# Kernel optimization log

Measured on AMD Instinct MI355X. Metric: run time of the kernel, lower is better.

## Reference

```python
import jax, jax.numpy as jnp
from jax import lax
import numpy as np

V, E, H, B, T = 512, 512, 1024, 128, 512

def _xavier(key, shape):
    fan_out, fan_in = shape
    bound = float(np.sqrt(6.0 / (fan_in + fan_out)))
    return jax.random.uniform(key, shape, jnp.float32, -bound, bound)

def setup_inputs() -> dict:
    key = jax.random.key(0)
    ks = jax.random.split(key, 6)
    src = jax.random.randint(ks[0], (B, T), 0, V, dtype=jnp.int32)
    embedding = _xavier(ks[1], (V, E))
    w_ih_l0 = _xavier(ks[2], (3 * H, E))
    w_hh_l0 = _xavier(ks[3], (3 * H, H))
    w_ih_l1 = _xavier(ks[4], (3 * H, H))
    w_hh_l1 = _xavier(ks[5], (3 * H, H))
    zb = jnp.zeros((3 * H,), jnp.float32)  # biases init'd to 0 in module
    return {
        "src": src, "embedding": embedding,
        "w_ih_l0": w_ih_l0, "w_hh_l0": w_hh_l0, "b_ih_l0": zb, "b_hh_l0": zb,
        "w_ih_l1": w_ih_l1, "w_hh_l1": w_hh_l1, "b_ih_l1": zb, "b_hh_l1": zb,
    }

def _gru_layer(x_seq, w_ih, w_hh, b_ih, b_hh):
    # x_seq: [B, T, D]. Precompute all input projections as one big GEMM.
    gates_x = jnp.einsum('btd,gd->btg', x_seq, w_ih) + b_ih  # [B, T, 3H]
    h_dim = w_hh.shape[1]
    w_hh_t = w_hh.T  # [H, 3H]

    def step(h, gx):
        gh = h @ w_hh_t + b_hh                      # [B, 3H]
        xr, xz, xn = jnp.split(gx, 3, axis=-1)
        hr, hz, hn = jnp.split(gh, 3, axis=-1)
        r = jax.nn.sigmoid(xr + hr)
        z = jax.nn.sigmoid(xz + hz)
        n = jnp.tanh(xn + r * hn)
        h_new = (1.0 - z) * n + z * h
        return h_new, h_new

    h0 = jnp.zeros((x_seq.shape[0], h_dim), x_seq.dtype)
    h_last, outs = lax.scan(step, h0, jnp.swapaxes(gates_x, 0, 1))  # time-major scan
    return jnp.swapaxes(outs, 0, 1), h_last  # [B, T, H], [B, H]

def reference(src, embedding, w_ih_l0, w_hh_l0, b_ih_l0, b_hh_l0,
              w_ih_l1, w_hh_l1, b_ih_l1, b_hh_l1):
    x = embedding[src]  # [B, T, E]
    y0, h0 = _gru_layer(x, w_ih_l0, w_hh_l0, b_ih_l0, b_hh_l0)
    _, h1 = _gru_layer(y0, w_ih_l1, w_hh_l1, b_ih_l1, b_hh_l1)
    return jnp.stack([h0, h1], axis=0)  # (n_layers, B, H)
```

## Files before the change

kernel.cpp:

```cpp
#include <hip/hip_runtime.h>

typedef __attribute__((ext_vector_type(8))) short short8;
typedef __attribute__((ext_vector_type(4))) float f32x4;

constexpr int Bsz = 128;
constexpr int Tlen = 512;
constexpr int Hd = 1024;
constexpr int RS = 128 * 1024;

__device__ __forceinline__ unsigned short f2b(float f) {
  unsigned int u = __float_as_uint(f);
  u = (u + 0x7FFFu + ((u >> 16) & 1u)) >> 16;
  return (unsigned short)u;
}
__device__ __forceinline__ unsigned int aload32(const unsigned int* p) {
  return __hip_atomic_load(p, __ATOMIC_RELAXED, __HIP_MEMORY_SCOPE_AGENT);
}
__device__ __forceinline__ void astore32(unsigned int* p, unsigned int v) {
  __hip_atomic_store(p, v, __ATOMIC_RELAXED, __HIP_MEMORY_SCOPE_AGENT);
}

template <int LAYER>
__device__ __forceinline__ void run_layer(
    const int* __restrict__ src, const float* __restrict__ P,
    const unsigned short* __restrict__ Wh, const unsigned short* __restrict__ Wx,
    const float* __restrict__ bhh, const float* __restrict__ bih,
    float* __restrict__ dout,
    unsigned short* __restrict__ A0r,
    unsigned short* __restrict__ A1hr,
    unsigned short* __restrict__ A1xr,
    unsigned int* __restrict__ flags,
    unsigned int* __restrict__ invflags,
    f32x4 (*__restrict__ red)[4][3][64],
    const int R0, const int J0, const int w, const int lane,
    const int tid, const int c, const int xcd, const bool isInv)
{
  constexpr int NQ = LAYER ? 4 : 3;
  const int lrow = lane >> 4;
  const int lcol = lane & 15;
  const int col = J0 + lcol;
  const int mh = R0 >> 6;
  const int dom = LAYER * 2 + mh;

  const float bhr = bhh[col], bhz = bhh[1024 + col], bhn = bhh[2048 + col];
  float gbr = 0.f, gbz = 0.f, gbn = 0.f;
  if (LAYER) { gbr = bih[col]; gbz = bih[1024 + col]; gbn = bih[2048 + col]; }

  short8 wBh[3][8];
#pragma unroll
  for (int g = 0; g < 3; ++g) {
    const unsigned short* wp = Wh + (g * 1024 + col) * 1024 + w * 256 + lrow * 8;
#pragma unroll
    for (int ks = 0; ks < 8; ++ks) wBh[g][ks] = *(const short8*)(wp + ks * 32);
  }
  short8 wBx[3][8];
  if (LAYER) {
#pragma unroll
    for (int g = 0; g < 3; ++g) {
      const unsigned short* wp = Wx + (g * 1024 + col) * 1024 + w * 256 + lrow * 8;
#pragma unroll
      for (int ks = 0; ks < 8; ++ks) wBx[g][ks] = *(const short8*)(wp + ks * 32);
    }
  }

  const int myrow0 = R0 + w * 16 + lrow * 4;
  float hold[4] = {0.f, 0.f, 0.f, 0.f};

  for (int r = 0; r <= 512; ++r) {
    if (LAYER == 0 && r == 512) break;
    const bool active = LAYER ? (r >= 1) : true;

    if (active) {
      const int scur = r & 3, snext = (r + 1) & 3;

      float gpr[4], gpz[4], gpn[4];
      if (LAYER == 0) {
        int sv[4];
#pragma unroll
        for (int i = 0; i < 4; ++i) sv[i] = src[(myrow0 + i) * Tlen + r];
#pragma unroll
        for (int i = 0; i < 4; ++i) {
          const float* pr = P + sv[i] * 3072 + col;
          gpr[i] = pr[0]; gpz[i] = pr[1024]; gpn[i] = pr[2048];
        }
      } else {
#pragma unroll
        for (int i = 0; i < 4; ++i) { gpr[i] = gbr; gpz[i] = gbz; gpn[i] = gbn; }
      }

      f32x4 ar[4], az[4], anh[4], anx[4];
#pragma unroll
      for (int f = 0; f < 4; ++f) {
        ar[f]  = (f32x4){0.f, 0.f, 0.f, 0.f};
        az[f]  = (f32x4){0.f, 0.f, 0.f, 0.f};
        anh[f] = (f32x4){0.f, 0.f, 0.f, 0.f};
        anx[f] = (f32x4){0.f, 0.f, 0.f, 0.f};
      }

      if (LAYER == 0) {
        if (r >= 1) {
          if (w == 0) {
            const unsigned tgt = (unsigned)r;
            if (isInv) {
              const unsigned tA = (r >= 2) ? (unsigned)(r - 2) : 0u;
              const unsigned int* f0 = flags + 0 * 64 + lane;
              const unsigned int* f1 = flags + 1 * 64 + lane;
              const unsigned int* f2 = flags + 2 * 64 + lane;
              const unsigned int* f3 = flags + 3 * 64 + lane;
              for (;;) {
                const unsigned a = aload32(f0), b = aload32(f1),
                               d = aload32(f2), e = aload32(f3);
                if (__all(a >= tgt && b >= tA && d >= tA && e >= tA)) break;
                __builtin_amdgcn_s_sleep(1);
              }
              __builtin_amdgcn_fence(__ATOMIC_ACQUIRE, "agent");
              if (lane == 0) astore32(&invflags[xcd * 16], (unsigned)(r + 1));
            } else {
              const unsigned int* fp = flags + mh * 64 + lane;
              const unsigned int* fs = flags + (2 + mh) * 64 + lane;
              const unsigned tgtS = (r >= 2) ? (unsigned)(r - 2) : 0u;
              const unsigned int* iv = &invflags[xcd * 16];
              for (;;) {
                const unsigned a = aload32(fp), b = aload32(fs), k = aload32(iv);
                if (__all(a >= tgt && b >= tgtS && k >= tgt)) break;
                __builtin_amdgcn_s_sleep(1);
              }
            }
          }
          __syncthreads();
          asm volatile("buffer_inv sc0" ::: "memory");

          const unsigned short* rb[4];
#pragma unroll
          for (int f = 0; f < 4; ++f)
            rb[f] = A0r + scur * RS + (R0 + f * 16 + lcol) * 1024 + w * 256 + lrow * 8;
          short8 ab[4][4];
#pragma unroll
          for (int s = 0; s < 4; ++s)
#pragma unroll
            for (int f = 0; f < 4; ++f) ab[s][f] = *(const short8*)(rb[f] + s * 32);
#pragma unroll
          for (int ks = 0; ks < 8; ++ks) {
#pragma unroll
            for (int f = 0; f < 4; ++f) {
              const short8 a = ab[ks & 3][f];
              ar[f]  = __builtin_amdgcn_mfma_f32_16x16x32_bf16(a, wBh[0][ks], ar[f], 0, 0, 0);
              az[f]  = __builtin_amdgcn_mfma_f32_16x16x32_bf16(a, wBh[1][ks], az[f], 0, 0, 0);
              anh[f] = __builtin_amdgcn_mfma_f32_16x16x32_bf16(a, wBh[2][ks], anh[f], 0, 0, 0);
            }
            if (ks + 4 < 8)
#pragma unroll
              for (int f = 0; f < 4; ++f)
                ab[ks & 3][f] = *(const short8*)(rb[f] + (ks + 4) * 32);
          }
        } else if (isInv) {
          if (w == 0 && lane == 0) astore32(&invflags[xcd * 16], 1u);
        }
      } else {
        if (w == 0) {
          const unsigned tgt = (unsigned)r;
          const unsigned int* fp = flags + mh * 64 + lane;
          const unsigned int* iv = &invflags[xcd * 16];
          for (;;) {
            const unsigned a = aload32(fp), k = aload32(iv);
            if (__all(a >= tgt && k >= tgt)) break;
            __builtin_amdgcn_s_sleep(1);
          }
        }
        __syncthreads();
        asm volatile("buffer_inv sc0" ::: "memory");
        {
          const unsigned short* rbx[4];
#pragma unroll
          for (int f = 0; f < 4; ++f)
            rbx[f] = A1xr + scur * RS + (R0 + f * 16 + lcol) * 1024 + w * 256 + lrow * 8;
          short8 ab[4][4];
#pragma unroll
          for (int s = 0; s < 4; ++s)
#pragma unroll
            for (int f = 0; f < 4; ++f) ab[s][f] = *(const short8*)(rbx[f] + s * 32);
#pragma unroll
          for (int ks = 0; ks < 8; ++ks) {
#pragma unroll
            for (int f = 0; f < 4; ++f) {
              const short8 a = ab[ks & 3][f];
              ar[f]  = __builtin_amdgcn_mfma_f32_16x16x32_bf16(a, wBx[0][ks], ar[f], 0, 0, 0);
              az[f]  = __builtin_amdgcn_mfma_f32_16x16x32_bf16(a, wBx[1][ks], az[f], 0, 0, 0);
              anx[f] = __builtin_amdgcn_mfma_f32_16x16x32_bf16(a, wBx[2][ks], anx[f], 0, 0, 0);
            }
            if (ks + 4 < 8)
#pragma unroll
              for (int f = 0; f < 4; ++f)
                ab[ks & 3][f] = *(const short8*)(rbx[f] + (ks + 4) * 32);
          }
        }
        if (r >= 2) {
          if (w == 0) {
            const unsigned tgt = (unsigned)r;
            const unsigned int* fs = flags + (2 + mh) * 64 + lane;
            for (;;) {
              const unsigned b = aload32(fs);
              if (__all(b >= tgt)) break;
              __builtin_amdgcn_s_sleep(1);
            }
          }
          __syncthreads();
          asm volatile("buffer_inv sc0" ::: "memory");
          const unsigned short* rbh[4];
#pragma unroll
          for (int f = 0; f < 4; ++f)
            rbh[f] = A1hr + scur * RS + (R0 + f * 16 + lcol) * 1024 + w * 256 + lrow * 8;
          short8 ab[4][4];
#pragma unroll
          for (int s = 0; s < 4; ++s)
#pragma unroll
            for (int f = 0; f < 4; ++f) ab[s][f] = *(const short8*)(rbh[f] + s * 32);
#pragma unroll
          for (int ks = 0; ks < 8; ++ks) {
#pragma unroll
            for (int f = 0; f < 4; ++f) {
              const short8 a = ab[ks & 3][f];
              ar[f]  = __builtin_amdgcn_mfma_f32_16x16x32_bf16(a, wBh[0][ks], ar[f], 0, 0, 0);
              az[f]  = __builtin_amdgcn_mfma_f32_16x16x32_bf16(a, wBh[1][ks], az[f], 0, 0, 0);
              anh[f] = __builtin_amdgcn_mfma_f32_16x16x32_bf16(a, wBh[2][ks], anh[f], 0, 0, 0);
            }
            if (ks + 4 < 8)
#pragma unroll
              for (int f = 0; f < 4; ++f)
                ab[ks & 3][f] = *(const short8*)(rbh[f] + (ks + 4) * 32);
          }
        }
      }

#pragma unroll
      for (int f = 0; f < 4; ++f) {
        if (f != w) {
          const int sl = (f < w) ? f : f - 1;
          red[w][0][sl][lane] = ar[f];
          red[w][1][sl][lane] = az[f];
          red[w][2][sl][lane] = anh[f];
          if (NQ == 4) red[w][3][sl][lane] = anx[f];
        }
      }
      __syncthreads();
      f32x4 sr  = (f32x4){0.f, 0.f, 0.f, 0.f};
      f32x4 sz_ = (f32x4){0.f, 0.f, 0.f, 0.f};
      f32x4 snh = (f32x4){0.f, 0.f, 0.f, 0.f};
      f32x4 snx = (f32x4){0.f, 0.f, 0.f, 0.f};
#pragma unroll
      for (int f = 0; f < 4; ++f)
        if (f == w) { sr = ar[f]; sz_ = az[f]; snh = anh[f]; if (NQ == 4) snx = anx[f]; }
#pragma unroll
      for (int ww = 0; ww < 4; ++ww) {
        if (ww != w) {
          const int sl = (w < ww) ? w : w - 1;
          sr  += red[ww][0][sl][lane];
          sz_ += red[ww][1][sl][lane];
          snh += red[ww][2][sl][lane];
          if (NQ == 4) snx += red[ww][3][sl][lane];
        }
      }

      const bool lastw = LAYER ? (r == 512) : (r == 511);
#pragma unroll
      for (int i = 0; i < 4; ++i) {
        const int row = myrow0 + i;
        float rg = sr[i] + gpr[i] + bhr;
        rg = 1.f / (1.f + __expf(-rg));
        float zg = sz_[i] + gpz[i] + bhz;
        zg = 1.f / (1.f + __expf(-zg));
        const float nx = (snx[i] + gpn[i]) + rg * (snh[i] + bhn);
        const float e2 = __expf(2.f * fabsf(nx));
        const float ng = copysignf(1.f - 2.f / (e2 + 1.f), nx);
        const float hnew = (1.f - zg) * ng + zg * hold[i];
        hold[i] = hnew;
        const unsigned int hb = (unsigned int)f2b(hnew);
        const unsigned int nb = (unsigned int)__shfl_down((int)hb, 1, 64);
        if ((lcol & 1) == 0) {
          const unsigned int pv = hb | (nb << 16);
          if (LAYER == 0) {
            astore32((unsigned int*)(A0r + snext * RS + row * 1024 + J0 + lcol), pv);
            astore32((unsigned int*)(A1xr + snext * RS + row * 1024 + J0 + lcol), pv);
          } else {
            astore32((unsigned int*)(A1hr + snext * RS + row * 1024 + J0 + lcol), pv);
          }
        }
        if (lastw) dout[LAYER * (Bsz * Hd) + row * Hd + col] = hnew;
      }
    }

    __syncthreads();
    if (tid == 0) astore32(&flags[dom * 64 + c], (unsigned)(r + 1));
  }
}

__global__ void __launch_bounds__(256, 1) gru_persist(
    const int* __restrict__ src,
    const float* __restrict__ P,
    const unsigned short* __restrict__ Whh0b,
    const unsigned short* __restrict__ Whh1b,
    const unsigned short* __restrict__ Wih1b,
    const float* __restrict__ bhh0,
    const float* __restrict__ bih1,
    const float* __restrict__ bhh1,
    float* __restrict__ dout,
    unsigned short* __restrict__ A0,
    unsigned short* __restrict__ A1h,
    unsigned short* __restrict__ A1x,
    unsigned int* __restrict__ flags,
    unsigned int* __restrict__ invflags,
    int* __restrict__ taken)
{
  __shared__ f32x4 red[4][4][3][64];
  __shared__ int s_work;

  const int tid = threadIdx.x;
  const int lane = tid & 63;

  if (tid == 0) {
    unsigned int xcc;
    asm volatile("s_getreg_b32 %0, hwreg(HW_REG_XCC_ID)" : "=s"(xcc));
    const int pref = ((int)(xcc & 7u)) * 32;
    int got = -1;
    for (int j = 0; j < 32 && got < 0; ++j) {
      const int idx = pref + j;
      int expected = 0;
      if (__hip_atomic_compare_exchange_strong(&taken[idx], &expected, 1,
              __ATOMIC_RELAXED, __ATOMIC_RELAXED, __HIP_MEMORY_SCOPE_AGENT))
        got = idx;
    }
    for (int j = 0; j < 256 && got < 0; ++j) {
      const int idx = (pref + j) & 255;
      int expected = 0;
      if (__hip_atomic_compare_exchange_strong(&taken[idx], &expected, 1,
              __ATOMIC_RELAXED, __ATOMIC_RELAXED, __HIP_MEMORY_SCOPE_AGENT))
        got = idx;
    }
    s_work = got;
  }
  __syncthreads();
  const int work = s_work;

  if (work < 0) {
    float h0 = 1.00f, h1 = 1.25f, h2 = 1.50f, h3 = 1.75f;
    float h4 = 2.00f, h5 = 2.25f, h6 = 2.50f, h7 = 2.75f;
    const float mm = 1.0000001f, ad = 0.0000003f;
    for (;;) {
#pragma unroll
      for (int i = 0; i < 256; ++i) {
        h0 = __builtin_fmaf(h0, mm, ad); h1 = __builtin_fmaf(h1, mm, ad);
        h2 = __builtin_fmaf(h2, mm, ad); h3 = __builtin_fmaf(h3, mm, ad);
        h4 = __builtin_fmaf(h4, mm, ad); h5 = __builtin_fmaf(h5, mm, ad);
        h6 = __builtin_fmaf(h6, mm, ad); h7 = __builtin_fmaf(h7, mm, ad);
      }
      asm volatile("" :: "v"(h0), "v"(h1), "v"(h2), "v"(h3),
                         "v"(h4), "v"(h5), "v"(h6), "v"(h7));
      const unsigned a = aload32(&flags[128 + lane]);
      const unsigned b = aload32(&flags[192 + lane]);
      if (__all(a >= 513u && b >= 513u)) break;
    }
    return;
  }

  const int xcd_w = work >> 5;
  const int slot = work & 31;
  const int layer = (slot >> 4) & 1;
  const int m = (slot >> 1) & 7;
  const int c = xcd_w * 8 + m;
  const int mh = slot & 1;
  const int R0 = mh * 64;
  const int J0 = c * 16;
  const bool isInv = (slot == 0);

  const int w = tid >> 6;

  if (layer == 0)
    run_layer<0>(src, P, Whh0b, Wih1b, bhh0, bih1, dout, A0, A1h, A1x,
                 flags, invflags, red, R0, J0, w, lane, tid, c, xcd_w, isInv);
  else
    run_layer<1>(src, P, Whh1b, Wih1b, bhh1, bih1, dout, A0, A1h, A1x,
                 flags, invflags, red, R0, J0, w, lane, tid, c, xcd_w, false);
}

__global__ void __launch_bounds__(256) cvt_k(const float* __restrict__ s,
                                            unsigned short* __restrict__ d, int n) {
  const int i = (blockIdx.x * 256 + threadIdx.x) * 8;
  if (i >= n) return;
  const float4 a = *(const float4*)(s + i);
  const float4 b = *(const float4*)(s + i + 4);
  short8 o;
  o[0] = (short)f2b(a.x); o[1] = (short)f2b(a.y);
  o[2] = (short)f2b(a.z); o[3] = (short)f2b(a.w);
  o[4] = (short)f2b(b.x); o[5] = (short)f2b(b.y);
  o[6] = (short)f2b(b.z); o[7] = (short)f2b(b.w);
  *(short8*)(d + i) = o;
}

__global__ void __launch_bounds__(256) pemb_k(const float* __restrict__ emb,
                                             const float* __restrict__ wih0,
                                             const float* __restrict__ bih0,
                                             float* __restrict__ P) {
  __shared__ float se[64 * 64];
  const int g = blockIdx.x * 256 + threadIdx.x;
  const int v0 = blockIdx.y * 64;
  float acc[64];
#pragma unroll
  for (int i = 0; i < 64; ++i) acc[i] = 0.f;
  for (int kb = 0; kb < 8; ++kb) {
    __syncthreads();
#pragma unroll
    for (int s = 0; s < 4; ++s) {
      const int idx = threadIdx.x + s * 256;
      const int vv = idx >> 4, k4 = (idx & 15) * 4;
      *(float4*)(se + vv * 64 + k4) =
          *(const float4*)(emb + (v0 + vv) * 512 + kb * 64 + k4);
    }
    __syncthreads();
    float4 wv[16];
#pragma unroll
    for (int j = 0; j < 16; ++j)
      wv[j] = *(const float4*)(wih0 + g * 512 + kb * 64 + j * 4);
    for (int vv = 0; vv < 64; ++vv) {
      const float* er = se + vv * 64;
      float s0 = acc[vv];
#pragma unroll
      for (int j = 0; j < 16; ++j) {
        const float4 e = *(const float4*)(er + j * 4);
        s0 += wv[j].x * e.x + wv[j].y * e.y + wv[j].z * e.z + wv[j].w * e.w;
      }
      acc[vv] = s0;
    }
  }
  const float bb = bih0[g];
  for (int vv = 0; vv < 64; ++vv) P[(v0 + vv) * 3072 + g] = acc[vv] + bb;
}

__global__ void zero_k(unsigned int* flags, int* taken, unsigned int* invflags) {
  const int i = threadIdx.x;
  flags[i] = 0u;
  taken[i] = 0;
  if (i < 128) invflags[i] = 0u;
}

extern "C" void kernel_launch(void* const* d_in, const int* in_sizes, int n_in,
                              void* d_out, int out_size, void* d_ws, size_t ws_size,
                              hipStream_t stream) {
  const int* src = (const int*)d_in[0];
  const float* emb = (const float*)d_in[1];
  const float* wih0 = (const float*)d_in[2];
  const float* whh0 = (const float*)d_in[3];
  const float* bih0 = (const float*)d_in[4];
  const float* bhh0 = (const float*)d_in[5];
  const float* wih1 = (const float*)d_in[6];
  const float* whh1 = (const float*)d_in[7];
  const float* bih1 = (const float*)d_in[8];
  const float* bhh1 = (const float*)d_in[9];
  float* dout = (float*)d_out;

  char* p = (char*)d_ws;
  unsigned short* A0    = (unsigned short*)p;
  unsigned short* A1h   = (unsigned short*)(p + 1048576);
  unsigned short* A1x   = (unsigned short*)(p + 2097152);
  unsigned short* Whh0b = (unsigned short*)(p + 3145728);
  unsigned short* Whh1b = (unsigned short*)(p + 9437184);
  unsigned short* Wih1b = (unsigned short*)(p + 15728640);
  float* P              = (float*)(p + 22020096);
  unsigned int* flags   = (unsigned int*)(p + 28311552);
  unsigned int* invflags= (unsigned int*)(p + 28312576);
  int* taken            = (int*)(p + 28313600);

  constexpr int NW = 3072 * 1024;
  hipLaunchKernelGGL(cvt_k, dim3(NW / (256 * 8)), dim3(256), 0, stream, whh0, Whh0b, NW);
  hipLaunchKernelGGL(cvt_k, dim3(NW / (256 * 8)), dim3(256), 0, stream, whh1, Whh1b, NW);
  hipLaunchKernelGGL(cvt_k, dim3(NW / (256 * 8)), dim3(256), 0, stream, wih1, Wih1b, NW);
  hipLaunchKernelGGL(pemb_k, dim3(12, 8), dim3(256), 0, stream, emb, wih0, bih0, P);
  hipLaunchKernelGGL(zero_k, dim3(1), dim3(256), 0, stream, flags, taken, invflags);

  hipLaunchKernelGGL(gru_persist, dim3(512), dim3(256), 0, stream,
                     src, P, Whh0b, Whh1b, Wih1b, bhh0, bih1, bhh1,
                     dout, A0, A1h, A1x, flags, invflags, taken);
}
```

Measured before the change: 9.115 ms.

## Spin all waves on flags with FMA burn instead of sleep+barrier; drop idle blocks

Each wave now polls the inter-block progress flags itself and spins with dependent FMA chains, replacing the single-wave poll with s_sleep followed by __syncthreads. The grid shrinks from 512 to 256 blocks, the idle filler blocks that burned ALU (apparently to hold clocks up) are removed, and the same-XCD first pass of work claiming is dropped. The aim is lower wake-up latency per recurrent step and no block-wide barrier, at the cost of more atomic polling traffic and more ALU use during spins.

```diff
diff --git a/kernel.cpp b/kernel.cpp
--- a/kernel.cpp
+++ b/kernel.cpp
@@ -19,6 +19,28 @@
 __device__ __forceinline__ void astore32(unsigned int* p, unsigned int v) {
   __hip_atomic_store(p, v, __ATOMIC_RELAXED, __HIP_MEMORY_SCOPE_AGENT);
 }
+
+#define BURN_DECL()                                                        \
+  float b0 = (float)lane + 2.0f, b1 = b0 + 0.37f, b2 = b0 + 0.71f,         \
+        b3 = b0 + 1.13f, b4 = b0 + 1.79f, b5 = b0 + 2.39f,                 \
+        b6 = b0 + 2.97f, b7 = b0 + 3.61f
+
+#define BURN8()                                                            \
+  do {                                                                     \
+    _Pragma("unroll")                                                      \
+    for (int _i = 0; _i < 16; ++_i) {                                      \
+      b0 = __builtin_fmaf(b0, 1.0000001f, 1e-7f);                          \
+      b1 = __builtin_fmaf(b1, 1.0000001f, 1e-7f);                          \
+      b2 = __builtin_fmaf(b2, 1.0000001f, 1e-7f);                          \
+      b3 = __builtin_fmaf(b3, 1.0000001f, 1e-7f);                          \
+      b4 = __builtin_fmaf(b4, 1.0000001f, 1e-7f);                          \
+      b5 = __builtin_fmaf(b5, 1.0000001f, 1e-7f);                          \
+      b6 = __builtin_fmaf(b6, 1.0000001f, 1e-7f);                          \
+      b7 = __builtin_fmaf(b7, 1.0000001f, 1e-7f);                          \
+    }                                                                      \
+    asm volatile("" : "+v"(b0), "+v"(b1), "+v"(b2), "+v"(b3),              \
+                      "+v"(b4), "+v"(b5), "+v"(b6), "+v"(b7));             \
+  } while (0)
 
 template <int LAYER>
 __device__ __forceinline__ void run_layer(
@@ -99,35 +121,34 @@
 
       if (LAYER == 0) {
         if (r >= 1) {
-          if (w == 0) {
-            const unsigned tgt = (unsigned)r;
-            if (isInv) {
-              const unsigned tA = (r >= 2) ? (unsigned)(r - 2) : 0u;
-              const unsigned int* f0 = flags + 0 * 64 + lane;
-              const unsigned int* f1 = flags + 1 * 64 + lane;
-              const unsigned int* f2 = flags + 2 * 64 + lane;
-              const unsigned int* f3 = flags + 3 * 64 + lane;
-              for (;;) {
-                const unsigned a = aload32(f0), b = aload32(f1),
-                               d = aload32(f2), e = aload32(f3);
-                if (__all(a >= tgt && b >= tA && d >= tA && e >= tA)) break;
-                __builtin_amdgcn_s_sleep(1);
-              }
-              __builtin_amdgcn_fence(__ATOMIC_ACQUIRE, "agent");
-              if (lane == 0) astore32(&invflags[xcd * 16], (unsigned)(r + 1));
-            } else {
-              const unsigned int* fp = flags + mh * 64 + lane;
-              const unsigned int* fs = flags + (2 + mh) * 64 + lane;
-              const unsigned tgtS = (r >= 2) ? (unsigned)(r - 2) : 0u;
-              const unsigned int* iv = &invflags[xcd * 16];
-              for (;;) {
-                const unsigned a = aload32(fp), b = aload32(fs), k = aload32(iv);
-                if (__all(a >= tgt && b >= tgtS && k >= tgt)) break;
-                __builtin_amdgcn_s_sleep(1);
-              }
-            }
-          }
-          __syncthreads();
+          const unsigned tgt = (unsigned)r;
+          if (isInv && w == 0) {
+            const unsigned tA = (r >= 2) ? (unsigned)(r - 2) : 0u;
+            const unsigned int* f0 = flags + lane;
+            const unsigned int* f1 = flags + 64 + lane;
+            const unsigned int* f2 = flags + 128 + lane;
+            const unsigned int* f3 = flags + 192 + lane;
+            BURN_DECL();
+            for (;;) {
+              const unsigned a = aload32(f0), b = aload32(f1),
+                             d = aload32(f2), e = aload32(f3);
+              if (__all(a >= tgt && b >= tA && d >= tA && e >= tA)) break;
+              BURN8();
+            }
+            __builtin_amdgcn_fence(__ATOMIC_ACQUIRE, "agent");
+            if (lane == 0) astore32(&invflags[xcd * 16], (unsigned)(r + 1));
+          } else {
+            const unsigned tS = (r >= 2) ? (unsigned)(r - 2) : 0u;
+            const unsigned int* fp = flags + mh * 64 + lane;
+            const unsigned int* fs = flags + (2 + mh) * 64 + lane;
+            const unsigned int* iv = &invflags[xcd * 16];
+            BURN_DECL();
+            for (;;) {
+              const unsigned a = aload32(fp), b = aload32(fs), k = aload32(iv);
+              if (__all(a >= tgt && b >= tS && k >= tgt)) break;
+              BURN8();
+            }
+          }
           asm volatile("buffer_inv sc0" ::: "memory");
 
           const unsigned short* rb[4];
@@ -157,17 +178,17 @@
           if (w == 0 && lane == 0) astore32(&invflags[xcd * 16], 1u);
         }
       } else {
-        if (w == 0) {
+        {
           const unsigned tgt = (unsigned)r;
           const unsigned int* fp = flags + mh * 64 + lane;
           const unsigned int* iv = &invflags[xcd * 16];
+          BURN_DECL();
           for (;;) {
             const unsigned a = aload32(fp), k = aload32(iv);
             if (__all(a >= tgt && k >= tgt)) break;
-            __builtin_amdgcn_s_sleep(1);
-          }
-        }
-        __syncthreads();
+            BURN8();
+          }
+        }
         asm volatile("buffer_inv sc0" ::: "memory");
         {
           const unsigned short* rbx[4];
@@ -195,16 +216,16 @@
           }
         }
         if (r >= 2) {
-          if (w == 0) {
+          {
             const unsigned tgt = (unsigned)r;
             const unsigned int* fs = flags + (2 + mh) * 64 + lane;
+            BURN_DECL();
             for (;;) {
               const unsigned b = aload32(fs);
               if (__all(b >= tgt)) break;
-              __builtin_amdgcn_s_sleep(1);
-            }
-          }
-          __syncthreads();
+              BURN8();
+            }
+          }
           asm volatile("buffer_inv sc0" ::: "memory");
           const unsigned short* rbh[4];
 #pragma unroll
@@ -322,13 +343,6 @@
     asm volatile("s_getreg_b32 %0, hwreg(HW_REG_XCC_ID)" : "=s"(xcc));
     const int pref = ((int)(xcc & 7u)) * 32;
     int got = -1;
-    for (int j = 0; j < 32 && got < 0; ++j) {
-      const int idx = pref + j;
-      int expected = 0;
-      if (__hip_atomic_compare_exchange_strong(&taken[idx], &expected, 1,
-              __ATOMIC_RELAXED, __ATOMIC_RELAXED, __HIP_MEMORY_SCOPE_AGENT))
-        got = idx;
-    }
     for (int j = 0; j < 256 && got < 0; ++j) {
       const int idx = (pref + j) & 255;
       int expected = 0;
@@ -340,28 +354,6 @@
   }
   __syncthreads();
   const int work = s_work;
-
-  if (work < 0) {
-    float h0 = 1.00f, h1 = 1.25f, h2 = 1.50f, h3 = 1.75f;
-    float h4 = 2.00f, h5 = 2.25f, h6 = 2.50f, h7 = 2.75f;
-    const float mm = 1.0000001f, ad = 0.0000003f;
-    for (;;) {
-#pragma unroll
-      for (int i = 0; i < 256; ++i) {
-        h0 = __builtin_fmaf(h0, mm, ad); h1 = __builtin_fmaf(h1, mm, ad);
-        h2 = __builtin_fmaf(h2, mm, ad); h3 = __builtin_fmaf(h3, mm, ad);
-        h4 = __builtin_fmaf(h4, mm, ad); h5 = __builtin_fmaf(h5, mm, ad);
-        h6 = __builtin_fmaf(h6, mm, ad); h7 = __builtin_fmaf(h7, mm, ad);
-      }
-      asm volatile("" :: "v"(h0), "v"(h1), "v"(h2), "v"(h3),
-                         "v"(h4), "v"(h5), "v"(h6), "v"(h7));
-      const unsigned a = aload32(&flags[128 + lane]);
-      const unsigned b = aload32(&flags[192 + lane]);
-      if (__all(a >= 513u && b >= 513u)) break;
-    }
-    return;
-  }
-
   const int xcd_w = work >> 5;
   const int slot = work & 31;
   const int layer = (slot >> 4) & 1;
@@ -476,7 +468,7 @@
   hipLaunchKernelGGL(pemb_k, dim3(12, 8), dim3(256), 0, stream, emb, wih0, bih0, P);
   hipLaunchKernelGGL(zero_k, dim3(1), dim3(256), 0, stream, flags, taken, invflags);
 
-  hipLaunchKernelGGL(gru_persist, dim3(512), dim3(256), 0, stream,
+  hipLaunchKernelGGL(gru_persist, dim3(256), dim3(256), 0, stream,
                      src, P, Whh0b, Whh1b, Wih1b, bhh0, bih1, bhh1,
                      dout, A0, A1h, A1x, flags, invflags, taken);
 }
```

New measurement: 9.272 ms. About the same (+1.7%).
